# Optimization experiments

Hardware: AMD Instinct MI355X
Metric: run time of the kernel (lower is better)

Reference implementation:

```python
import jax, jax.numpy as jnp
import numpy as np

B, N, C = 8, 16384, 40
E, KD, VD = 512, 256, 256


def setup_inputs() -> dict:
    key = jax.random.key(0)
    ks = jax.random.split(key, 10)
    s = 0.02
    return {
        "q": jax.random.normal(ks[0], (B, N, E), jnp.float32),
        "k": jax.random.normal(ks[1], (B, C, KD), jnp.float32),
        "v": jax.random.normal(ks[2], (B, C, VD), jnp.float32),
        "coarse_pred": jax.random.normal(ks[3], (B, C, N), jnp.float32),
        "Wq": jax.random.normal(ks[4], (E, E), jnp.float32) * s,
        "bq": jnp.zeros((E,), jnp.float32),
        "Wk": jax.random.normal(ks[5], (E, KD), jnp.float32) * s,
        "bk": jnp.zeros((E,), jnp.float32),
        "Wv": jax.random.normal(ks[6], (E, VD), jnp.float32) * s,
        "bv": jnp.zeros((E,), jnp.float32),
    }


def reference(q, k, v, coarse_pred, Wq, bq, Wk, bk, Wv, bv):
    # Projections (nn.Linear: x @ W.T + b)
    qp = jnp.einsum("bne,fe->bnf", q, Wq) + bq          # (B, N, E)
    kp = jnp.einsum("bcd,fd->bcf", k, Wk) + bk          # (B, C, E)
    vp = jnp.einsum("bcd,fd->bcf", v, Wv) + bv          # (B, C, E)

    scale = 1.0 / jnp.sqrt(jnp.float32(E))
    attn = jnp.einsum("bne,bce->bnc", qp, kp) * scale   # (B, N, C)
    attn = jax.nn.softmax(attn, axis=-1)

    # coarse_pred is detached, transposed to (B, N, C), softmaxed over classes
    cp = jax.nn.softmax(jnp.swapaxes(coarse_pred, 1, 2), axis=-1)
    attn = jax.nn.softmax(attn * cp, axis=-1)

    out = jnp.einsum("bnc,bce->bne", attn, vp)          # (B, N, E)
    return out
```

## Files before the change

kernel.cpp:

```cpp
#include <hip/hip_runtime.h>
#include <hip/hip_bf16.h>
#include <stdint.h>

#define Bb 8
#define Nn 16384
#define Cc 40
#define Ee 512
#define Dd 256

typedef __attribute__((ext_vector_type(4))) float f32x4;
typedef __attribute__((ext_vector_type(8))) short bf16x8;

__device__ __forceinline__ unsigned short f2bf(float f) {
  union { float f; uint32_t u; } x; x.f = f;
  uint32_t r = x.u + 0x7FFFu + ((x.u >> 16) & 1u);
  return (unsigned short)(r >> 16);
}
__device__ __forceinline__ unsigned int pack2(float a, float b) {
  return (unsigned int)f2bf(a) | ((unsigned int)f2bf(b) << 16);
}
__device__ __forceinline__ bf16x8 q2bf(float4 a, float4 c) {
  union { __hip_bfloat162 h2[4]; bf16x8 v; } u;
  u.h2[0] = __float22bfloat162_rn(float2{a.x, a.y});
  u.h2[1] = __float22bfloat162_rn(float2{a.z, a.w});
  u.h2[2] = __float22bfloat162_rn(float2{c.x, c.y});
  u.h2[3] = __float22bfloat162_rn(float2{c.z, c.w});
  return u.v;
}

__global__ __launch_bounds__(256) void prepA_kernel(
    const float* __restrict__ Wq, const float* __restrict__ Wk,
    const float* __restrict__ bq, const float* __restrict__ bk,
    float* __restrict__ Mt, float* __restrict__ tvec,
    float* __restrict__ uvec, float* __restrict__ bqbk) {
  const int t = threadIdx.x;
  if (blockIdx.x == 8) {
    if (blockIdx.z != 0) return;
    const int by = blockIdx.y;
    if (by < 2) {
      const int e = by * 256 + t;
      float s = 0.f;
      #pragma unroll 8
      for (int f = 0; f < Ee; f++) s += Wq[(size_t)f * Ee + e] * bk[f];
      tvec[e] = s;
    } else if (by == 2) {
      const int d = t;
      float s = 0.f;
      #pragma unroll 8
      for (int f = 0; f < Ee; f++) s += Wk[(size_t)f * Dd + d] * bq[f];
      uvec[d] = s;
    } else {
      __shared__ float red[256];
      float p = 0.f;
      for (int f = t; f < Ee; f += 256) p += bq[f] * bk[f];
      red[t] = p; __syncthreads();
      #pragma unroll
      for (int off = 128; off > 0; off >>= 1) {
        if (t < off) red[t] += red[t + off];
        __syncthreads();
      }
      if (t == 0) bqbk[0] = red[0];
    }
    return;
  }
  __shared__ float WqL[64][68];
  __shared__ float WkL[64][68];
  const int te = (t & 15) * 4;
  const int td = (t >> 4) * 4;
  const int ebase = blockIdx.x * 64, dbase = blockIdx.y * 64;
  const int fbase = blockIdx.z * 256;
  f32x4 acc0 = {0,0,0,0}, acc1 = {0,0,0,0}, acc2 = {0,0,0,0}, acc3 = {0,0,0,0};
  for (int f0 = 0; f0 < 256; f0 += 64) {
    __syncthreads();
    #pragma unroll
    for (int i = 0; i < 4; i++) {
      int idx = t + i * 256;
      int row = idx >> 4, c4 = (idx & 15) * 4;
      *(float4*)&WqL[row][c4] = *(const float4*)(Wq + (size_t)(fbase + f0 + row) * Ee + ebase + c4);
      *(float4*)&WkL[row][c4] = *(const float4*)(Wk + (size_t)(fbase + f0 + row) * Dd + dbase + c4);
    }
    __syncthreads();
    #pragma unroll 8
    for (int ff = 0; ff < 64; ff++) {
      float4 a = *(const float4*)&WkL[ff][td];
      float4 b = *(const float4*)&WqL[ff][te];
      acc0[0] += a.x*b.x; acc0[1] += a.x*b.y; acc0[2] += a.x*b.z; acc0[3] += a.x*b.w;
      acc1[0] += a.y*b.x; acc1[1] += a.y*b.y; acc1[2] += a.y*b.z; acc1[3] += a.y*b.w;
      acc2[0] += a.z*b.x; acc2[1] += a.z*b.y; acc2[2] += a.z*b.z; acc2[3] += a.z*b.w;
      acc3[0] += a.w*b.x; acc3[1] += a.w*b.y; acc3[2] += a.w*b.z; acc3[3] += a.w*b.w;
    }
  }
  float* mt = Mt + (size_t)blockIdx.z * 131072;
  *(f32x4*)&mt[(size_t)(dbase + td + 0) * Ee + ebase + te] = acc0;
  *(f32x4*)&mt[(size_t)(dbase + td + 1) * Ee + ebase + te] = acc1;
  *(f32x4*)&mt[(size_t)(dbase + td + 2) * Ee + ebase + te] = acc2;
  *(f32x4*)&mt[(size_t)(dbase + td + 3) * Ee + ebase + te] = acc3;
}

__global__ __launch_bounds__(256) void prepB_kernel(
    const float* __restrict__ k, const float* __restrict__ v,
    const float* __restrict__ Wv, const float* __restrict__ bv,
    const float* __restrict__ Mt, const float* __restrict__ tvec,
    const float* __restrict__ uvec, const float* __restrict__ bqbk,
    unsigned short* __restrict__ abf, unsigned short* __restrict__ vpf,
    float* __restrict__ dbias) {
  __shared__ float xL[8][Dd];
  const int t = threadIdx.x;
  const int el = t & 127, half = t >> 7;
  const int e = blockIdx.y * 128 + el;

  if (blockIdx.x < 48) {
    const int sbase = blockIdx.x * 8;
    for (int i = t; i < 8 * Dd; i += 256) {
      int row = i >> 8, dd = i & (Dd - 1);
      int sg = sbase + row, bb_ = sg / 48, cc = sg % 48;
      xL[row][dd] = (cc < 40) ? k[((size_t)bb_ * Cc + cc) * Dd + dd] : 0.f;
    }
    __syncthreads();
    float acc[4] = {0,0,0,0};
    float db[4]  = {0,0,0,0};
    #pragma unroll 8
    for (int d = 0; d < Dd; d++) {
      float mt = Mt[(size_t)d * Ee + e] + Mt[131072 + (size_t)d * Ee + e];
      float ud = uvec[d];
      #pragma unroll
      for (int si = 0; si < 4; si++) {
        float kv = xL[half*4 + si][d];
        acc[si] += mt * kv;
        db[si]  += ud * kv;
      }
    }
    const float scale = 0.044194173824159216f;
    const float te = tvec[e];
    const float bqbkv = bqbk[0];
    const int ks = e >> 5, gg = (e >> 3) & 3, j = e & 7;
    #pragma unroll
    for (int si = 0; si < 4; si++) {
      int sg = sbase + half*4 + si, bb_ = sg / 48, cc = sg % 48;
      int ct = cc >> 4, lane16 = (cc & 15) + 16*gg;
      unsigned short val = (cc < 40) ? f2bf(scale * (acc[si] + te)) : (unsigned short)0;
      abf[((((size_t)bb_*3 + ct)*16 + ks)*64 + lane16)*8 + j] = val;
      if (el == 0) dbias[bb_*64 + cc] = (cc < 40) ? scale * (db[si] + bqbkv) : 0.f;
    }
  } else {
    const int sbase = (blockIdx.x - 48) * 8;
    for (int i = t; i < 8 * Dd; i += 256) {
      int row = i >> 8, dd = i & (Dd - 1);
      int sg = sbase + row, bb_ = sg >> 6, cc = sg & 63;
      xL[row][dd] = (cc < 40) ? v[((size_t)bb_ * Cc + cc) * Dd + dd] : 0.f;
    }
    __syncthreads();
    const float* wrow = Wv + (size_t)e * Dd;
    float acc[4] = {0,0,0,0};
    #pragma unroll 2
    for (int dd = 0; dd < Dd; dd += 4) {
      float4 w = *(const float4*)(wrow + dd);
      #pragma unroll
      for (int si = 0; si < 4; si++) {
        float4 vv = *(const float4*)&xL[half*4 + si][dd];
        acc[si] += w.x*vv.x + w.y*vv.y + w.z*vv.z + w.w*vv.w;
      }
    }
    const float bve = bv[e];
    const int nt = e >> 4, elan = e & 15;
    #pragma unroll
    for (int si = 0; si < 4; si++) {
      int sg = sbase + half*4 + si, bb_ = sg >> 6, cc = sg & 63;
      int s = cc >> 5, gg = (cc >> 3) & 3, j = cc & 7;
      unsigned short val = (cc < 40) ? f2bf(acc[si] + bve) : (unsigned short)0;
      vpf[((((size_t)bb_*32 + nt)*2 + s)*64 + (elan + 16*gg))*8 + j] = val;
    }
  }
}

__global__ __launch_bounds__(1024) void main_kernel(
    const float* __restrict__ q, const float* __restrict__ coarse,
    const unsigned short* __restrict__ abfrag,
    const unsigned short* __restrict__ vpfrag,
    const float* __restrict__ dbias, float* __restrict__ out) {
  __shared__ uint4 fragL[7168];
  __shared__ unsigned short s_att[16][16][72];
  const int t = threadIdx.x;
  const int wave = t >> 6, lane = t & 63;
  const int r = lane & 15, g = lane >> 4;
  const int b = blockIdx.x >> 5;
  const int seg = blockIdx.x & 31;
  const bool v2 = (g < 2);

  {
    const uint4* srcA = (const uint4*)abfrag + (size_t)b * 3072;
    #pragma unroll
    for (int i = 0; i < 3; i++) fragL[t + i*1024] = srcA[t + i*1024];
    const uint4* srcV = (const uint4*)vpfrag + (size_t)b * 4096;
    #pragma unroll
    for (int i = 0; i < 4; i++) fragL[3072 + t + i*1024] = srcV[t + i*1024];
  }
  __syncthreads();

  const int row0 = seg * 512 + wave * 16;
  const float* qrow0 = q + ((size_t)b * Nn + row0 + r) * Ee + 8 * g;
  const float* cbase0 = coarse + (size_t)b * Cc * Nn + row0 + r;
  float* outb0 = out + ((size_t)b * Nn + row0 + r) * Ee + 4 * g;

  for (int it = 0; it < 2; it++) {
    const float* qr = qrow0 + (size_t)(it*256) * Ee;
    f32x4 acc0 = {0,0,0,0}, acc1 = {0,0,0,0}, acc2 = {0,0,0,0};

    const float* cb = cbase0 + it*256;
    float cr[3][4];
    #pragma unroll
    for (int rg = 0; rg < 4; rg++) {
      cr[0][rg] = cb[(size_t)( 0 + 4*g + rg) * Nn];
      cr[1][rg] = cb[(size_t)(16 + 4*g + rg) * Nn];
      cr[2][rg] = v2 ? cb[(size_t)(32 + 4*g + rg) * Nn] : -3e38f;
    }

    float4 a0, a1, b0, b1;
    auto LD_A = [&](int c) {
      a0 = *(const float4*)(qr + 32*c);
      a1 = *(const float4*)(qr + 32*c + 4);
    };
    auto LD_B = [&](int c) {
      b0 = *(const float4*)(qr + 32*c);
      b1 = *(const float4*)(qr + 32*c + 4);
    };
    auto MM = [&](int ks, float4 x0, float4 x1) {
      bf16x8 qf = q2bf(x0, x1);
      acc0 = __builtin_amdgcn_mfma_f32_16x16x32_bf16(*(const bf16x8*)&fragL[(0*16+ks)*64 + lane], qf, acc0, 0,0,0);
      acc1 = __builtin_amdgcn_mfma_f32_16x16x32_bf16(*(const bf16x8*)&fragL[(1*16+ks)*64 + lane], qf, acc1, 0,0,0);
      acc2 = __builtin_amdgcn_mfma_f32_16x16x32_bf16(*(const bf16x8*)&fragL[(2*16+ks)*64 + lane], qf, acc2, 0,0,0);
    };

    LD_A(0); LD_B(1);
    MM( 0, a0, a1); LD_A( 2);
    MM( 1, b0, b1); LD_B( 3);
    MM( 2, a0, a1); LD_A( 4);
    MM( 3, b0, b1); LD_B( 5);
    MM( 4, a0, a1); LD_A( 6);
    MM( 5, b0, b1); LD_B( 7);
    MM( 6, a0, a1); LD_A( 8);
    MM( 7, b0, b1); LD_B( 9);
    MM( 8, a0, a1); LD_A(10);
    MM( 9, b0, b1); LD_B(11);
    MM(10, a0, a1); LD_A(12);
    MM(11, b0, b1); LD_B(13);
    MM(12, a0, a1); LD_A(14);
    MM(13, b0, b1); LD_B(15);
    MM(14, a0, a1);
    MM(15, b0, b1);

    const float4 db0 = *(const float4*)(dbias + b*64 +  0 + 4*g);
    const float4 db1 = *(const float4*)(dbias + b*64 + 16 + 4*g);
    const float4 db2 = *(const float4*)(dbias + b*64 + 32 + 4*g);

    float x[3][4];
    #pragma unroll
    for (int rg = 0; rg < 4; rg++) {
      x[0][rg] = acc0[rg] + ((const float*)&db0)[rg];
      x[1][rg] = acc1[rg] + ((const float*)&db1)[rg];
      x[2][rg] = acc2[rg] + ((const float*)&db2)[rg];
    }

    float m1 = -3e38f;
    #pragma unroll
    for (int rg = 0; rg < 4; rg++) {
      m1 = fmaxf(m1, x[0][rg]); m1 = fmaxf(m1, x[1][rg]);
      if (v2) m1 = fmaxf(m1, x[2][rg]);
    }
    m1 = fmaxf(m1, __shfl_xor(m1, 16));
    m1 = fmaxf(m1, __shfl_xor(m1, 32));
    float s1 = 0.f;
    #pragma unroll
    for (int rg = 0; rg < 4; rg++) {
      x[0][rg] = __expf(x[0][rg] - m1); s1 += x[0][rg];
      x[1][rg] = __expf(x[1][rg] - m1); s1 += x[1][rg];
      x[2][rg] = v2 ? __expf(x[2][rg] - m1) : 0.f; s1 += x[2][rg];
    }
    s1 += __shfl_xor(s1, 16); s1 += __shfl_xor(s1, 32);

    float m2 = -3e38f;
    #pragma unroll
    for (int rg = 0; rg < 4; rg++) {
      m2 = fmaxf(m2, cr[0][rg]); m2 = fmaxf(m2, cr[1][rg]);
      if (v2) m2 = fmaxf(m2, cr[2][rg]);
    }
    m2 = fmaxf(m2, __shfl_xor(m2, 16));
    m2 = fmaxf(m2, __shfl_xor(m2, 32));
    float s2 = 0.f;
    #pragma unroll
    for (int rg = 0; rg < 4; rg++) {
      cr[0][rg] = __expf(cr[0][rg] - m2); s2 += cr[0][rg];
      cr[1][rg] = __expf(cr[1][rg] - m2); s2 += cr[1][rg];
      cr[2][rg] = v2 ? __expf(cr[2][rg] - m2) : 0.f; s2 += cr[2][rg];
    }
    s2 += __shfl_xor(s2, 16); s2 += __shfl_xor(s2, 32);

    const float sc12 = 1.0f / (s1 * s2);
    float m3 = -3e38f;
    #pragma unroll
    for (int rg = 0; rg < 4; rg++) {
      x[0][rg] *= cr[0][rg] * sc12;
      x[1][rg] *= cr[1][rg] * sc12;
      x[2][rg] = v2 ? (x[2][rg] * cr[2][rg] * sc12) : 0.f;
      m3 = fmaxf(m3, x[0][rg]); m3 = fmaxf(m3, x[1][rg]);
      if (v2) m3 = fmaxf(m3, x[2][rg]);
    }
    m3 = fmaxf(m3, __shfl_xor(m3, 16));
    m3 = fmaxf(m3, __shfl_xor(m3, 32));
    float s3 = 0.f;
    #pragma unroll
    for (int rg = 0; rg < 4; rg++) {
      x[0][rg] = __expf(x[0][rg] - m3); s3 += x[0][rg];
      x[1][rg] = __expf(x[1][rg] - m3); s3 += x[1][rg];
      x[2][rg] = v2 ? __expf(x[2][rg] - m3) : 0.f; s3 += x[2][rg];
    }
    s3 += __shfl_xor(s3, 16); s3 += __shfl_xor(s3, 32);
    const float inv3 = 1.0f / s3;

    unsigned int* srow = (unsigned int*)&s_att[wave][r][0];
    #pragma unroll
    for (int ct = 0; ct < 3; ct++) {
      srow[8*ct + 2*g + 0] = pack2(x[ct][0]*inv3, x[ct][1]*inv3);
      srow[8*ct + 2*g + 1] = pack2(x[ct][2]*inv3, x[ct][3]*inv3);
    }
    srow[24 + 2*g + 0] = 0u;
    srow[24 + 2*g + 1] = 0u;
    asm volatile("s_waitcnt lgkmcnt(0)" ::: "memory");
    const bf16x8 pa0 = *(const bf16x8*)&s_att[wave][r][ 0 + 8*g];
    const bf16x8 pa1 = *(const bf16x8*)&s_att[wave][r][32 + 8*g];

    float* outp = outb0 + (size_t)(it*256) * Ee;
    #pragma unroll 8
    for (int nt = 0; nt < 32; nt++) {
      bf16x8 vf0 = *(const bf16x8*)&fragL[3072 + (nt*2 + 0)*64 + lane];
      bf16x8 vf1 = *(const bf16x8*)&fragL[3072 + (nt*2 + 1)*64 + lane];
      f32x4 o = {0,0,0,0};
      o = __builtin_amdgcn_mfma_f32_16x16x32_bf16(vf0, pa0, o, 0,0,0);
      o = __builtin_amdgcn_mfma_f32_16x16x32_bf16(vf1, pa1, o, 0,0,0);
      *(f32x4*)(outp + nt*16) = o;
    }
  }
}

extern "C" void kernel_launch(void* const* d_in, const int* in_sizes, int n_in,
                              void* d_out, int out_size, void* d_ws, size_t ws_size,
                              hipStream_t stream) {
  const float* q   = (const float*)d_in[0];
  const float* k   = (const float*)d_in[1];
  const float* v   = (const float*)d_in[2];
  const float* cps = (const float*)d_in[3];
  const float* Wq  = (const float*)d_in[4];
  const float* bq  = (const float*)d_in[5];
  const float* Wk  = (const float*)d_in[6];
  const float* bk  = (const float*)d_in[7];
  const float* Wv  = (const float*)d_in[8];
  const float* bv  = (const float*)d_in[9];
  float* out = (float*)d_out;
  char* ws = (char*)d_ws;

  float*          Mt    = (float*)(ws);
  float*          tvec  = (float*)(ws + 1048576);
  float*          uvec  = (float*)(ws + 1050624);
  float*          bqbkp = (float*)(ws + 1051648);
  unsigned short* abf   = (unsigned short*)(ws + 1052672);
  unsigned short* vpf   = (unsigned short*)(ws + 1052672 + 393216);
  float*          dbias = (float*)(ws + 1052672 + 393216 + 524288);

  prepA_kernel<<<dim3(9, 4, 2), 256, 0, stream>>>(Wq, Wk, bq, bk, Mt, tvec, uvec, bqbkp);
  prepB_kernel<<<dim3(112, 4),  256, 0, stream>>>(k, v, Wv, bv, Mt, tvec, uvec, bqbkp,
                                                  abf, vpf, dbias);
  main_kernel <<<dim3(256),    1024, 0, stream>>>(q, cps, abf, vpf, dbias, out);
}
```

Before: 175.0 us.

## Split fused attention kernel into score/softmax and PV-output kernels

The single fused kernel is split in two. The first computes the Q·K scores and the double softmax, then writes bf16 attention weights in MFMA fragment layout to workspace. The second loads the V fragments into shared memory and runs the PV matmul to write the fp32 output. Each kernel uses 512-thread blocks over 512 blocks with less shared memory, which should raise occupancy and let the read-heavy and write-heavy phases each run better. The cost is an extra launch and a round trip of the attention weights through global memory.

```diff
diff --git a/kernel.cpp b/kernel.cpp
--- a/kernel.cpp
+++ b/kernel.cpp
@@ -173,40 +173,32 @@
   }
 }
 
-__global__ __launch_bounds__(1024) void main_kernel(
+__global__ __launch_bounds__(512) void main1_kernel(
     const float* __restrict__ q, const float* __restrict__ coarse,
     const unsigned short* __restrict__ abfrag,
-    const unsigned short* __restrict__ vpfrag,
-    const float* __restrict__ dbias, float* __restrict__ out) {
-  __shared__ uint4 fragL[7168];
-  __shared__ unsigned short s_att[16][16][72];
+    const float* __restrict__ dbias, unsigned short* __restrict__ attw) {
+  __shared__ uint4 abL[3072];
+  __shared__ unsigned short s_att[8][16][72];
   const int t = threadIdx.x;
   const int wave = t >> 6, lane = t & 63;
   const int r = lane & 15, g = lane >> 4;
-  const int b = blockIdx.x >> 5;
-  const int seg = blockIdx.x & 31;
+  const int b = blockIdx.x >> 6;
+  const int seg = blockIdx.x & 63;
   const bool v2 = (g < 2);
 
   {
     const uint4* srcA = (const uint4*)abfrag + (size_t)b * 3072;
     #pragma unroll
-    for (int i = 0; i < 3; i++) fragL[t + i*1024] = srcA[t + i*1024];
-    const uint4* srcV = (const uint4*)vpfrag + (size_t)b * 4096;
-    #pragma unroll
-    for (int i = 0; i < 4; i++) fragL[3072 + t + i*1024] = srcV[t + i*1024];
+    for (int i = 0; i < 6; i++) abL[t + i*512] = srcA[t + i*512];
   }
   __syncthreads();
 
-  const int row0 = seg * 512 + wave * 16;
-  const float* qrow0 = q + ((size_t)b * Nn + row0 + r) * Ee + 8 * g;
-  const float* cbase0 = coarse + (size_t)b * Cc * Nn + row0 + r;
-  float* outb0 = out + ((size_t)b * Nn + row0 + r) * Ee + 4 * g;
-
   for (int it = 0; it < 2; it++) {
-    const float* qr = qrow0 + (size_t)(it*256) * Ee;
+    const int row0 = seg * 256 + it * 128 + wave * 16;
+    const float* qr = q + ((size_t)b * Nn + row0 + r) * Ee + 8 * g;
     f32x4 acc0 = {0,0,0,0}, acc1 = {0,0,0,0}, acc2 = {0,0,0,0};
 
-    const float* cb = cbase0 + it*256;
+    const float* cb = coarse + (size_t)b * Cc * Nn + row0 + r;
     float cr[3][4];
     #pragma unroll
     for (int rg = 0; rg < 4; rg++) {
@@ -226,9 +218,9 @@
     };
     auto MM = [&](int ks, float4 x0, float4 x1) {
       bf16x8 qf = q2bf(x0, x1);
-      acc0 = __builtin_amdgcn_mfma_f32_16x16x32_bf16(*(const bf16x8*)&fragL[(0*16+ks)*64 + lane], qf, acc0, 0,0,0);
-      acc1 = __builtin_amdgcn_mfma_f32_16x16x32_bf16(*(const bf16x8*)&fragL[(1*16+ks)*64 + lane], qf, acc1, 0,0,0);
-      acc2 = __builtin_amdgcn_mfma_f32_16x16x32_bf16(*(const bf16x8*)&fragL[(2*16+ks)*64 + lane], qf, acc2, 0,0,0);
+      acc0 = __builtin_amdgcn_mfma_f32_16x16x32_bf16(*(const bf16x8*)&abL[(0*16+ks)*64 + lane], qf, acc0, 0,0,0);
+      acc1 = __builtin_amdgcn_mfma_f32_16x16x32_bf16(*(const bf16x8*)&abL[(1*16+ks)*64 + lane], qf, acc1, 0,0,0);
+      acc2 = __builtin_amdgcn_mfma_f32_16x16x32_bf16(*(const bf16x8*)&abL[(2*16+ks)*64 + lane], qf, acc2, 0,0,0);
     };
 
     LD_A(0); LD_B(1);
@@ -329,11 +321,40 @@
     const bf16x8 pa0 = *(const bf16x8*)&s_att[wave][r][ 0 + 8*g];
     const bf16x8 pa1 = *(const bf16x8*)&s_att[wave][r][32 + 8*g];
 
-    float* outp = outb0 + (size_t)(it*256) * Ee;
+    const size_t aidx = (size_t)b * 1024 + (row0 >> 4);
+    *(bf16x8*)(attw + (aidx*2 + 0)*512 + lane*8) = pa0;
+    *(bf16x8*)(attw + (aidx*2 + 1)*512 + lane*8) = pa1;
+  }
+}
+
+__global__ __launch_bounds__(512) void main2_kernel(
+    const unsigned short* __restrict__ attw,
+    const unsigned short* __restrict__ vpfrag, float* __restrict__ out) {
+  __shared__ uint4 vpL[4096];
+  const int t = threadIdx.x;
+  const int wave = t >> 6, lane = t & 63;
+  const int r = lane & 15, g = lane >> 4;
+  const int b = blockIdx.x >> 6;
+  const int seg = blockIdx.x & 63;
+
+  {
+    const uint4* srcV = (const uint4*)vpfrag + (size_t)b * 4096;
+    #pragma unroll
+    for (int i = 0; i < 8; i++) vpL[t + i*512] = srcV[t + i*512];
+  }
+  __syncthreads();
+
+  for (int it = 0; it < 2; it++) {
+    const int row0 = seg * 256 + it * 128 + wave * 16;
+    const size_t aidx = (size_t)b * 1024 + (row0 >> 4);
+    const bf16x8 pa0 = *(const bf16x8*)(attw + (aidx*2 + 0)*512 + lane*8);
+    const bf16x8 pa1 = *(const bf16x8*)(attw + (aidx*2 + 1)*512 + lane*8);
+
+    float* outp = out + ((size_t)b * Nn + row0 + r) * Ee + 4 * g;
     #pragma unroll 8
     for (int nt = 0; nt < 32; nt++) {
-      bf16x8 vf0 = *(const bf16x8*)&fragL[3072 + (nt*2 + 0)*64 + lane];
-      bf16x8 vf1 = *(const bf16x8*)&fragL[3072 + (nt*2 + 1)*64 + lane];
+      bf16x8 vf0 = *(const bf16x8*)&vpL[(nt*2 + 0)*64 + lane];
+      bf16x8 vf1 = *(const bf16x8*)&vpL[(nt*2 + 1)*64 + lane];
       f32x4 o = {0,0,0,0};
       o = __builtin_amdgcn_mfma_f32_16x16x32_bf16(vf0, pa0, o, 0,0,0);
       o = __builtin_amdgcn_mfma_f32_16x16x32_bf16(vf1, pa1, o, 0,0,0);
@@ -365,9 +386,11 @@
   unsigned short* abf   = (unsigned short*)(ws + 1052672);
   unsigned short* vpf   = (unsigned short*)(ws + 1052672 + 393216);
   float*          dbias = (float*)(ws + 1052672 + 393216 + 524288);
+  unsigned short* attw  = (unsigned short*)(ws + 1052672 + 393216 + 524288 + 2048);
 
   prepA_kernel<<<dim3(9, 4, 2), 256, 0, stream>>>(Wq, Wk, bq, bk, Mt, tvec, uvec, bqbkp);
   prepB_kernel<<<dim3(112, 4),  256, 0, stream>>>(k, v, Wv, bv, Mt, tvec, uvec, bqbkp,
                                                   abf, vpf, dbias);
-  main_kernel <<<dim3(256),    1024, 0, stream>>>(q, cps, abf, vpf, dbias, out);
-}
+  main1_kernel<<<dim3(512),     512, 0, stream>>>(q, cps, abf, dbias, attw);
+  main2_kernel<<<dim3(512),     512, 0, stream>>>(attw, vpf, out);
+}
```

Result: slower. 190.0 us (+8.6%).
